# Optimization experiments

Hardware: AMD Instinct MI355X
Metric: run time of the kernel (lower is better)

## Reference

```python
import jax, jax.numpy as jnp
import numpy as np

B, T, S, A, P = 256, 32, 2048, 64, 128


def setup_inputs() -> dict:
    key = jax.random.key(0)
    ks = jax.random.split(key, 10)
    def w(k, shape, fan_in):
        return jax.random.normal(k, shape, dtype=jnp.float32) / np.sqrt(fan_in)
    return {
        "state": jax.random.normal(ks[0], (B, S), dtype=jnp.float32),
        "act_sequence": jax.random.normal(ks[1], (B, T, A), dtype=jnp.float32),
        "latent": jax.random.normal(ks[2], (B, P), dtype=jnp.float32),
        "fc_W": w(ks[3], (S, S + A + P), S + A + P),
        "fc_b": jnp.zeros((S,), dtype=jnp.float32),
        "fc1_W": w(ks[4], (S, 2 * S), 2 * S),
        "fc2_W": w(ks[5], (S, S), S),
        "W_W": w(ks[6], (4 * S, S), S),
        "reward_W": w(ks[7], (1, S), S),
        "reward_b": jnp.zeros((1,), dtype=jnp.float32),
    }


def reference(state, act_sequence, latent, fc_W, fc_b, fc1_W, fc2_W, W_W, reward_W, reward_b):
    s_dim = fc2_W.shape[0]
    relu = jax.nn.relu

    def fc(x):  # nn.Linear(s+a+p -> s, bias=True)
        return x @ fc_W.T + fc_b

    # initial hidden/cell both from relu(fc(cat[state, act[:,0], latent]))
    hs0 = jnp.concatenate([state, act_sequence[:, 0, :], latent], axis=1)
    hidden = relu(fc(hs0))
    cell = relu(fc(hs0))

    acts = jnp.transpose(act_sequence, (1, 0, 2))  # [T, B, A]

    def step(carry, act_i):
        h, c = carry
        # LSTMCell called as lstm(hidden, [hidden, cell]) -> input == h_cur == h
        combined = jnp.concatenate([h, h], axis=1)            # [B, 2S]
        x = relu(combined @ fc1_W.T)
        x = relu(x @ fc2_W.T)
        cc = relu(x @ W_W.T)                                   # [B, 4S]
        cc_i, cc_f, cc_o, cc_g = jnp.split(cc, 4, axis=1)
        i_g = jax.nn.sigmoid(cc_i)
        f_g = jax.nn.sigmoid(cc_f)
        o_g = jax.nn.sigmoid(cc_o)
        g_g = jnp.tanh(cc_g)
        c_next = f_g * c + i_g * g_g
        h_next = o_g * jnp.tanh(c_next)
        reward = h_next @ reward_W.T + reward_b                # [B, 1]
        # hidden for next iteration (uses act_sequence[:, i, :], as in source);
        # at the last step this carry is simply discarded.
        hs = jnp.concatenate([h_next, act_i, latent], axis=1)
        h_carry = relu(fc(hs))
        return (h_carry, c_next), (h_next, reward)

    (_, _), (preds, rewards) = jax.lax.scan(step, (hidden, cell), acts)
    # torch.cat(list, dim=0) over T steps of [B, *] -> [T*B, *]
    preds = preds.reshape(-1, s_dim)
    rewards = rewards.reshape(-1, 1)
    return preds, rewards
```

## Files before the change

### kernel.cpp

```cpp
#include <hip/hip_runtime.h>

typedef unsigned short u16;
typedef unsigned int   u32;
typedef __attribute__((ext_vector_type(8))) short s8v;
typedef __attribute__((ext_vector_type(8))) unsigned short u8v;
typedef __attribute__((ext_vector_type(4))) unsigned short u4h;
typedef __attribute__((ext_vector_type(4))) float f32x4;

__device__ __forceinline__ float bf2f(u16 v) {
    union { u32 u; float f; } x; x.u = ((u32)v) << 16; return x.f;
}
__device__ __forceinline__ u16 f2bf(float f) {
    union { float f; u32 u; } x; x.f = f;
    return (u16)((x.u + 0x7fffu + ((x.u >> 16) & 1u)) >> 16);
}
__device__ __forceinline__ float sigf(float x)  { return 1.0f / (1.0f + __expf(-x)); }
__device__ __forceinline__ float tanhf_(float x){ return 1.0f - 2.0f / (__expf(2.0f * x) + 1.0f); }

constexpr int Bb = 256, Tt = 32, Ss = 2048, Aa = 64, Pp = 128, SAPd = 2240;

typedef const __attribute__((address_space(1))) unsigned int* gp1_t;
typedef __attribute__((address_space(3))) unsigned int* lp3_t;
__device__ __forceinline__ void gl16(const void* g, void* l) {
    __builtin_amdgcn_global_load_lds((gp1_t)g, (lp3_t)l, 16, 0, 0);
}
#define VMWAIT(n) asm volatile("s_waitcnt vmcnt(" #n ")" ::: "memory")

template<int NBXPX, int NBY>
__device__ __forceinline__ void xcd_decode(int& bx, int& by) {
    int id  = blockIdx.x;
    int xcd = id & 7, i = id >> 3;
    bx = xcd * NBXPX + (i & (NBXPX - 1));
    by = i / NBXPX;
}

__global__ void detect_k(const u32* __restrict__ st, int* __restrict__ flag) {
    u32 w = st[threadIdx.x];
    int e = (w >> 7) & 0xFF;
    unsigned long long m = __ballot(e >= 100 && e <= 140);
    if (threadIdx.x == 0) flag[0] = (__popcll(m) >= 32) ? 1 : 0;
}

__global__ __launch_bounds__(256)
void prep_k(const void* __restrict__ state, const void* __restrict__ act,
            const void* __restrict__ latent, const void* __restrict__ fc1W,
            u16* __restrict__ hs, u16* __restrict__ fc1s, float* __restrict__ rewbuf,
            const int* __restrict__ flagp, int big)
{
    const bool bfe = (flagp[0] == 1);
    int g0 = blockIdx.x * 256 + threadIdx.x;
    int stride = gridDim.x * 256;
    for (int i = g0; i < Bb * SAPd; i += stride) {
        int b = i / SAPd, k = i - b * SAPd;
        const void* p; size_t src;
        if (k < Ss)           { p = state;  src = (size_t)b * Ss + k; }
        else if (k < Ss + Aa) { p = act;    src = (size_t)b * (Tt * Aa) + (k - Ss); }
        else                  { p = latent; src = (size_t)b * Pp + (k - Ss - Aa); }
        hs[i] = bfe ? ((const u16*)p)[src] : f2bf(((const float*)p)[src]);
    }
    for (int i = g0; i < Tt * Bb; i += stride) rewbuf[i] = 0.0f;
    if (big) {
        for (int i = g0; i < Ss * Ss; i += stride) {
            int n = i >> 11, k = i & 2047;
            float s;
            if (bfe) s = bf2f(((const u16*)fc1W)[(size_t)n * 4096 + k])
                       + bf2f(((const u16*)fc1W)[(size_t)n * 4096 + 2048 + k]);
            else     s = ((const float*)fc1W)[(size_t)n * 4096 + k]
                       + ((const float*)fc1W)[(size_t)n * 4096 + 2048 + k];
            fc1s[i] = f2bf(s);
        }
    }
}

template<int K, bool BIAS, bool WC, bool FOLD, bool ACT, bool WBF>
__global__ __launch_bounds__(256)
void gemm_k(const u16* __restrict__ Ap, const void* __restrict__ Wp,
            const void* __restrict__ biasp, u16* __restrict__ outp,
            float* __restrict__ cellp,
            u16* __restrict__ hsp, const void* __restrict__ actp, int t,
            const int* __restrict__ flagp)
{
    constexpr int NK = K / 64;
    __shared__ __align__(16) char smem[36864 + 8192];
    const bool bfe = (flagp[0] == 1);
    const int tid = threadIdx.x;
    const int lane = tid & 63, w = tid >> 6, m16 = lane & 15, q = lane >> 4;
    const int ct = w & 1, khw = w >> 1;
    int bx, by; xcd_decode<4, 8>(bx, by);
    const int r0 = by * 32, c0 = bx * 64;

    if (ACT) {
        if (by == 0) {
            int i = bx * 512 + tid * 2;
            int b = i >> 6, a2 = i & 63;
            if (bfe) {
                u32 v = *(const u32*)((const u16*)actp + ((size_t)b * Tt + t) * Aa + a2);
                *(u32*)(hsp + (size_t)b * SAPd + Ss + a2) = v;
            } else {
                const float* s = (const float*)actp + ((size_t)b * Tt + t) * Aa + a2;
                *(u32*)(hsp + (size_t)b * SAPd + Ss + a2) =
                    (u32)f2bf(s[0]) | ((u32)f2bf(s[1]) << 16);
            }
            VMWAIT(0);
        }
    }

    const int srow = tid >> 3, sch = tid & 7;
    const int fr2 = 32 + srow;
    f32x4 acc[4] = {};
    const bool mainp = (WBF || bfe) && !FOLD;

    auto COMPUTE = [&](int p) {
        const char* bufA = smem + p * 12288;
        const char* bufB = bufA + 4096;
        const int sw = (m16 & 7) << 4;
        const int cb = ((khw << 6) | (q << 4)) ^ sw;
        s8v a0 = *(const s8v*)(bufA + m16 * 128 + cb);
        s8v a1 = *(const s8v*)(bufA + (16 + m16) * 128 + cb);
        s8v b0 = *(const s8v*)(bufB + (ct * 32 + m16) * 128 + cb);
        s8v b1 = *(const s8v*)(bufB + (ct * 32 + 16 + m16) * 128 + cb);
        acc[0] = __builtin_amdgcn_mfma_f32_16x16x32_bf16(a0, b0, acc[0], 0, 0, 0);
        acc[1] = __builtin_amdgcn_mfma_f32_16x16x32_bf16(a1, b0, acc[1], 0, 0, 0);
        acc[2] = __builtin_amdgcn_mfma_f32_16x16x32_bf16(a0, b1, acc[2], 0, 0, 0);
        acc[3] = __builtin_amdgcn_mfma_f32_16x16x32_bf16(a1, b1, acc[3], 0, 0, 0);
    };

    if (mainp) {
        const u16* W16 = (const u16*)Wp;
        auto STAGE = [&](int kt, int p) {
            char* bufA = smem + p * 12288;
            char* bufB = bufA + 4096;
            int kb = kt * 64;
            gl16(Ap + (size_t)(r0 + srow) * K + kb + ((sch ^ (srow & 7)) * 8),
                 bufA + w * 1024);
            gl16(W16 + (size_t)(c0 + srow) * K + kb + ((sch ^ (srow & 7)) * 8),
                 bufB + w * 1024);
            gl16(W16 + (size_t)(c0 + fr2) * K + kb + ((sch ^ (fr2 & 7)) * 8),
                 bufB + 4096 + w * 1024);
        };
        STAGE(0, 0); STAGE(1, 1);
        for (int k = 0; k < NK - 2; k++) {
            VMWAIT(3);
            __builtin_amdgcn_s_barrier();
            STAGE(k + 2, (k + 2) % 3);
            COMPUTE(k % 3);
        }
        VMWAIT(3);
        __builtin_amdgcn_s_barrier();
        COMPUTE((NK - 2) % 3);
        VMWAIT(0);
        __builtin_amdgcn_s_barrier();
        COMPUTE((NK - 1) % 3);
    } else {
        u8v fa; u8v rbh[4]; float4 rff[8];
        auto ISSUE = [&](int kt) {
            int kb = kt * 64;
            fa = *(const u8v*)(Ap + (size_t)(r0 + srow) * K + kb + sch * 8);
            if (FOLD) {
                if (bfe) {
                    const u16* p1 = (const u16*)Wp + (size_t)(c0 + srow) * (2 * K) + kb + sch * 8;
                    rbh[0] = *(const u8v*)p1; rbh[1] = *(const u8v*)(p1 + K);
                    const u16* p2 = (const u16*)Wp + (size_t)(c0 + fr2) * (2 * K) + kb + sch * 8;
                    rbh[2] = *(const u8v*)p2; rbh[3] = *(const u8v*)(p2 + K);
                } else {
                    const float* p1 = (const float*)Wp + (size_t)(c0 + srow) * (2 * K) + kb + sch * 8;
                    rff[0] = *(const float4*)p1;       rff[1] = *(const float4*)(p1 + 4);
                    rff[2] = *(const float4*)(p1 + K); rff[3] = *(const float4*)(p1 + K + 4);
                    const float* p2 = (const float*)Wp + (size_t)(c0 + fr2) * (2 * K) + kb + sch * 8;
                    rff[4] = *(const float4*)p2;       rff[5] = *(const float4*)(p2 + 4);
                    rff[6] = *(const float4*)(p2 + K); rff[7] = *(const float4*)(p2 + K + 4);
                }
            } else {
                const float* p1 = (const float*)Wp + (size_t)(c0 + srow) * K + kb + sch * 8;
                rff[0] = *(const float4*)p1; rff[1] = *(const float4*)(p1 + 4);
                const float* p2 = (const float*)Wp + (size_t)(c0 + fr2) * K + kb + sch * 8;
                rff[2] = *(const float4*)p2; rff[3] = *(const float4*)(p2 + 4);
            }
        };
        auto COMMIT = [&](int p) {
            char* bufA = smem + p * 12288;
            char* bufB = bufA + 4096;
            *(u8v*)(bufA + srow * 128 + ((sch ^ (srow & 7)) * 16)) = fa;
            u8v v1, v2;
            if (FOLD) {
                if (bfe) {
                    #pragma unroll
                    for (int j = 0; j < 8; j++) {
                        v1[j] = f2bf(bf2f(rbh[0][j]) + bf2f(rbh[1][j]));
                        v2[j] = f2bf(bf2f(rbh[2][j]) + bf2f(rbh[3][j]));
                    }
                } else {
                    float a0[8], a1[8], b0[8], b1[8];
                    *(float4*)&a0[0] = rff[0]; *(float4*)&a0[4] = rff[1];
                    *(float4*)&a1[0] = rff[2]; *(float4*)&a1[4] = rff[3];
                    *(float4*)&b0[0] = rff[4]; *(float4*)&b0[4] = rff[5];
                    *(float4*)&b1[0] = rff[6]; *(float4*)&b1[4] = rff[7];
                    #pragma unroll
                    for (int j = 0; j < 8; j++) {
                        v1[j] = f2bf(a0[j] + a1[j]);
                        v2[j] = f2bf(b0[j] + b1[j]);
                    }
                }
            } else {
                float a0[8], a1[8];
                *(float4*)&a0[0] = rff[0]; *(float4*)&a0[4] = rff[1];
                *(float4*)&a1[0] = rff[2]; *(float4*)&a1[4] = rff[3];
                #pragma unroll
                for (int j = 0; j < 8; j++) { v1[j] = f2bf(a0[j]); v2[j] = f2bf(a1[j]); }
            }
            *(u8v*)(bufB + srow * 128 + ((sch ^ (srow & 7)) * 16)) = v1;
            *(u8v*)(bufB + fr2 * 128 + ((sch ^ (fr2 & 7)) * 16)) = v2;
        };
        ISSUE(0);
        for (int k = 0; k < NK; k++) {
            __syncthreads();
            COMMIT(k & 1);
            __syncthreads();
            if (k + 1 < NK) ISSUE(k + 1);
            COMPUTE(k & 1);
        }
    }

    f32x4* red = (f32x4*)(smem + 36864);
    if (khw == 1) {
        #pragma unroll
        for (int f = 0; f < 4; f++) red[(ct * 4 + f) * 64 + lane] = acc[f];
    }
    __syncthreads();
    if (khw == 0) {
        #pragma unroll
        for (int f = 0; f < 4; f++) acc[f] += red[(ct * 4 + f) * 64 + lane];
        #pragma unroll
        for (int cf = 0; cf < 2; cf++) {
            const int col = c0 + ct * 32 + cf * 16 + m16;
            float bv = 0.0f;
            if (BIAS) bv = bfe ? bf2f(((const u16*)biasp)[col]) : ((const float*)biasp)[col];
            #pragma unroll
            for (int af = 0; af < 2; af++) {
                f32x4 a = acc[cf * 2 + af];
                #pragma unroll
                for (int r = 0; r < 4; r++) {
                    int row = r0 + af * 16 + q * 4 + r;
                    float v = fmaxf(a[r] + bv, 0.0f);
                    outp[(size_t)row * 2048 + col] = f2bf(v);
                    if (WC) cellp[(size_t)row * 2048 + col] = v;
                }
            }
        }
    }
}

__global__ __launch_bounds__(256)
void wgates_k(const u16* __restrict__ Ap, const void* __restrict__ Wp,
              float* __restrict__ cbuf, u16* __restrict__ hsp,
              void* __restrict__ dout, const void* __restrict__ rwWp,
              float* __restrict__ rewbuf, int t, const int* __restrict__ flagp)
{
    constexpr int K = 2048, NK = 32;
    __shared__ __align__(16) char smem[49152];
    const bool bfe = (flagp[0] == 1);
    const int tid = threadIdx.x;
    const int lane = tid & 63, w = tid >> 6, m16 = lane & 15, q = lane >> 4;
    const int mi = w & 1, khw = w >> 1;
    int bx, by; xcd_decode<16, 4>(bx, by);
    const int r0 = by * 64, j0 = bx * 16;

    const int srow8 = lane >> 3, sch = lane & 7;
    f32x4 acc[8] = {};

    auto COMPUTE = [&](int p) {
        const char* bufA = smem + p * 16384;
        const char* bufB = bufA + 8192;
        const int sw = (m16 & 7) << 4;
        const int cb = ((khw << 6) | (q << 4)) ^ sw;
        s8v a0 = *(const s8v*)(bufA + (mi * 32 + m16) * 128 + cb);
        s8v a1 = *(const s8v*)(bufA + (mi * 32 + 16 + m16) * 128 + cb);
        #pragma unroll
        for (int cf = 0; cf < 4; cf++) {
            s8v b = *(const s8v*)(bufB + (cf * 16 + m16) * 128 + cb);
            acc[cf * 2 + 0] = __builtin_amdgcn_mfma_f32_16x16x32_bf16(a0, b, acc[cf * 2 + 0], 0, 0, 0);
            acc[cf * 2 + 1] = __builtin_amdgcn_mfma_f32_16x16x32_bf16(a1, b, acc[cf * 2 + 1], 0, 0, 0);
        }
    };

    if (bfe) {
        const u16* W16 = (const u16*)Wp;
        auto STAGE = [&](int kt, int p) {
            char* bufA = smem + p * 16384;
            char* bufB = bufA + 8192;
            int kb = kt * 64;
            #pragma unroll
            for (int i = 0; i < 2; i++) {
                int s = w * 2 + i;
                int row = s * 8 + srow8;
                int cg = sch ^ (row & 7);
                gl16(Ap + (size_t)(r0 + row) * K + kb + cg * 8, bufA + s * 1024);
            }
            #pragma unroll
            for (int i = 0; i < 2; i++) {
                int s = w * 2 + i;
                int row = s * 8 + srow8;
                int wr = (row >> 4) * 2048 + j0 + (row & 15);
                int cg = sch ^ (row & 7);
                gl16(W16 + (size_t)wr * K + kb + cg * 8, bufB + s * 1024);
            }
        };
        STAGE(0, 0); STAGE(1, 1);
        for (int k = 0; k < NK - 2; k++) {
            VMWAIT(4);
            __builtin_amdgcn_s_barrier();
            STAGE(k + 2, (k + 2) % 3);
            COMPUTE(k % 3);
        }
        VMWAIT(4);
        __builtin_amdgcn_s_barrier();
        COMPUTE((NK - 2) % 3);
        VMWAIT(0);
        __builtin_amdgcn_s_barrier();
        COMPUTE((NK - 1) % 3);
    } else {
        float4 rff[4];
        auto ISSUE = [&](int kt) {
            int kb = kt * 64;
            #pragma unroll
            for (int i = 0; i < 2; i++) {
                int slot = tid + i * 256;
                int brow = slot >> 3, bch = slot & 7;
                int wr = (brow >> 4) * 2048 + j0 + (brow & 15);
                int cg = bch ^ (brow & 7);
                const float* p1 = (const float*)Wp + (size_t)wr * K + kb + cg * 8;
                rff[2 * i] = *(const float4*)p1; rff[2 * i + 1] = *(const float4*)(p1 + 4);
            }
        };
        auto STAGE_A = [&](int kt, int p) {
            char* bufA = smem + p * 16384;
            int kb = kt * 64;
            #pragma unroll
            for (int i = 0; i < 2; i++) {
                int s = w * 2 + i;
                int row = s * 8 + srow8;
                int cg = sch ^ (row & 7);
                gl16(Ap + (size_t)(r0 + row) * K + kb + cg * 8, bufA + s * 1024);
            }
        };
        auto COMMIT = [&](int p) {
            char* bufB = smem + p * 16384 + 8192;
            #pragma unroll
            for (int i = 0; i < 2; i++) {
                int slot = tid + i * 256;
                int brow = slot >> 3, bch = slot & 7;
                float a0[8];
                *(float4*)&a0[0] = rff[2 * i]; *(float4*)&a0[4] = rff[2 * i + 1];
                u8v v;
                #pragma unroll
                for (int j = 0; j < 8; j++) v[j] = f2bf(a0[j]);
                *(u8v*)(bufB + brow * 128 + bch * 16) = v;
            }
        };
        ISSUE(0); STAGE_A(0, 0);
        for (int k = 0; k < NK; k++) {
            __syncthreads();
            COMMIT(k & 1);
            __syncthreads();
            if (k + 1 < NK) { STAGE_A(k + 1, (k + 1) & 1); ISSUE(k + 1); }
            COMPUTE(k & 1);
        }
    }

    f32x4* red = (f32x4*)(smem + 32768);
    if (khw == 1) {
        #pragma unroll
        for (int f = 0; f < 8; f++) red[(mi * 8 + f) * 64 + lane] = acc[f];
    }
    __syncthreads();
    float* gbuf = (float*)(smem + 32768);
    if (khw == 0) {
        #pragma unroll
        for (int f = 0; f < 8; f++) acc[f] += red[(mi * 8 + f) * 64 + lane];
        #pragma unroll
        for (int af = 0; af < 2; af++)
            #pragma unroll
            for (int r = 0; r < 4; r++) {
                int row = mi * 32 + af * 16 + q * 4 + r;
                f32x4 gv;
                #pragma unroll
                for (int cf = 0; cf < 4; cf++) gv[cf] = fmaxf(acc[cf * 2 + af][r], 0.0f);
                ((f32x4*)gbuf)[row * 16 + m16] = gv;
            }
    }
    __syncthreads();

    const int row = tid >> 2, jq = (tid & 3) * 4;
    const int grow = r0 + row, jcol = j0 + jq;
    float4 cold = *(const float4*)&cbuf[(size_t)grow * 2048 + jcol];
    float coldv[4] = { cold.x, cold.y, cold.z, cold.w };
    float rw4[4];
    #pragma unroll
    for (int u = 0; u < 4; u++)
        rw4[u] = bfe ? bf2f(((const u16*)rwWp)[jcol + u]) : ((const float*)rwWp)[jcol + u];

    float cn[4], hnf[4]; u4h hv;
    float rsum = 0.0f;
    #pragma unroll
    for (int u = 0; u < 4; u++) {
        const float* gq = &gbuf[((row * 16) + jq + u) * 4];
        float ig = sigf(gq[0]), fg = sigf(gq[1]), og = sigf(gq[2]), tg = tanhf_(gq[3]);
        float c_ = fg * coldv[u] + ig * tg;
        float hn = og * tanhf_(c_);
        cn[u] = c_; hnf[u] = hn; hv[u] = f2bf(hn);
        rsum += hn * rw4[u];
    }
    *(float4*)&cbuf[(size_t)grow * 2048 + jcol] = *(float4*)cn;
    *(u4h*)&hsp[(size_t)grow * SAPd + jcol] = hv;
    size_t pb = ((size_t)t * 256 + grow) * 2048 + jcol;
    if (bfe) *(u4h*)&((u16*)dout)[pb] = hv;
    else {
        #pragma unroll
        for (int u = 0; u < 4; u++) ((float*)dout)[pb + u] = hnf[u];
    }

    rsum += __shfl_xor(rsum, 1);
    rsum += __shfl_xor(rsum, 2);
    if ((tid & 3) == 0) atomicAdd(&rewbuf[t * 256 + grow], rsum);
}

__global__ void rewfin_k(const float* __restrict__ rewbuf, void* __restrict__ dout,
                         const void* __restrict__ rwb, const int* __restrict__ flagp) {
    const bool bfe = (flagp[0] == 1);
    int i = blockIdx.x * 256 + threadIdx.x;
    float rb = bfe ? bf2f(((const u16*)rwb)[0]) : ((const float*)rwb)[0];
    float v = rewbuf[i] + rb;
    size_t o = (size_t)Tt * Bb * Ss + i;
    if (bfe) ((u16*)dout)[o] = f2bf(v);
    else     ((float*)dout)[o] = v;
}

extern "C" void kernel_launch(void* const* d_in, const int* in_sizes, int n_in,
                              void* d_out, int out_size, void* d_ws, size_t ws_size,
                              hipStream_t stream)
{
    const void* state  = d_in[0];
    const void* act    = d_in[1];
    const void* latent = d_in[2];
    const void* fcW    = d_in[3];
    const void* fcb    = d_in[4];
    const void* fc1W   = d_in[5];
    const void* fc2W   = d_in[6];
    const void* WW     = d_in[7];
    const void* rwW    = d_in[8];
    const void* rwb    = d_in[9];
    char* ws = (char*)d_ws;

    int*   flag   = (int*)  (ws + 0);
    u16*   hs     = (u16*)  (ws + 1024);
    u16*   h      = (u16*)  (ws + 1147904);
    u16*   x1     = (u16*)  (ws + 2196480);
    u16*   x2     = (u16*)  (ws + 3245056);
    float* cbuf   = (float*)(ws + 4293632);
    float* rewbuf = (float*)(ws + 6390784);
    u16*   fc1s   = (u16*)  (ws + 6423552);
    const bool big = ws_size >= 14812160ull;

    detect_k<<<dim3(1), dim3(64), 0, stream>>>((const u32*)state, flag);
    prep_k<<<dim3(4096), dim3(256), 0, stream>>>(state, act, latent, fc1W,
                                                 hs, fc1s, rewbuf, flag, big ? 1 : 0);

    gemm_k<2240, true, true, false, false, false><<<dim3(256), dim3(256), 0, stream>>>(
        hs, fcW, fcb, h, cbuf, nullptr, nullptr, 0, flag);

    for (int t = 0; t < 32; t++) {
        if (big)
            gemm_k<2048, false, false, false, true, true><<<dim3(256), dim3(256), 0, stream>>>(
                h, fc1s, nullptr, x1, nullptr, hs, act, t, flag);
        else
            gemm_k<2048, false, false, true, true, false><<<dim3(256), dim3(256), 0, stream>>>(
                h, fc1W, nullptr, x1, nullptr, hs, act, t, flag);
        gemm_k<2048, false, false, false, false, false><<<dim3(256), dim3(256), 0, stream>>>(
            x1, fc2W, nullptr, x2, nullptr, nullptr, nullptr, 0, flag);
        wgates_k<<<dim3(512), dim3(256), 0, stream>>>(
            x2, WW, cbuf, hs, d_out, rwW, rewbuf, t, flag);
        if (t < 31)
            gemm_k<2240, true, false, false, false, false><<<dim3(256), dim3(256), 0, stream>>>(
                hs, fcW, fcb, h, nullptr, nullptr, nullptr, 0, flag);
    }
    rewfin_k<<<dim3(32), dim3(256), 0, stream>>>(rewbuf, d_out, rwb, flag);
}
```

Before: 2.708 ms.

## Enlarge wgates tile to 128 rows per block and drop split-K reduction

The gate GEMM kernel now processes 128 batch rows per block (256 blocks instead of 512), with each wave owning 32 rows over the full K chunk instead of splitting K across wave pairs. This halves the number of times each W_W tile is loaded across blocks and removes the LDS split-K reduction pass. The epilogue handles 8 columns per thread and does fewer atomics. In exchange it needs more LDS (72KB), doubles per-wave MFMA work per stage, and leaves only 256 blocks, which may reduce occupancy and latency hiding.

```diff
diff --git a/kernel.cpp b/kernel.cpp
--- a/kernel.cpp
+++ b/kernel.cpp
@@ -257,41 +257,43 @@
               float* __restrict__ rewbuf, int t, const int* __restrict__ flagp)
 {
     constexpr int K = 2048, NK = 32;
-    __shared__ __align__(16) char smem[49152];
+    __shared__ __align__(16) char smem[73728];
     const bool bfe = (flagp[0] == 1);
     const int tid = threadIdx.x;
     const int lane = tid & 63, w = tid >> 6, m16 = lane & 15, q = lane >> 4;
-    const int mi = w & 1, khw = w >> 1;
-    int bx, by; xcd_decode<16, 4>(bx, by);
-    const int r0 = by * 64, j0 = bx * 16;
+    int bx, by; xcd_decode<16, 2>(bx, by);
+    const int r0 = by * 128, j0 = bx * 16;
 
     const int srow8 = lane >> 3, sch = lane & 7;
     f32x4 acc[8] = {};
 
     auto COMPUTE = [&](int p) {
-        const char* bufA = smem + p * 16384;
-        const char* bufB = bufA + 8192;
+        const char* bufA = smem + p * 24576;
+        const char* bufB = bufA + 16384;
         const int sw = (m16 & 7) << 4;
-        const int cb = ((khw << 6) | (q << 4)) ^ sw;
-        s8v a0 = *(const s8v*)(bufA + (mi * 32 + m16) * 128 + cb);
-        s8v a1 = *(const s8v*)(bufA + (mi * 32 + 16 + m16) * 128 + cb);
-        #pragma unroll
-        for (int cf = 0; cf < 4; cf++) {
-            s8v b = *(const s8v*)(bufB + (cf * 16 + m16) * 128 + cb);
-            acc[cf * 2 + 0] = __builtin_amdgcn_mfma_f32_16x16x32_bf16(a0, b, acc[cf * 2 + 0], 0, 0, 0);
-            acc[cf * 2 + 1] = __builtin_amdgcn_mfma_f32_16x16x32_bf16(a1, b, acc[cf * 2 + 1], 0, 0, 0);
+        #pragma unroll
+        for (int kh = 0; kh < 2; kh++) {
+            const int cb = ((kh << 6) | (q << 4)) ^ sw;
+            s8v a0 = *(const s8v*)(bufA + (w * 32 + m16) * 128 + cb);
+            s8v a1 = *(const s8v*)(bufA + (w * 32 + 16 + m16) * 128 + cb);
+            #pragma unroll
+            for (int cf = 0; cf < 4; cf++) {
+                s8v b = *(const s8v*)(bufB + (cf * 16 + m16) * 128 + cb);
+                acc[cf * 2 + 0] = __builtin_amdgcn_mfma_f32_16x16x32_bf16(a0, b, acc[cf * 2 + 0], 0, 0, 0);
+                acc[cf * 2 + 1] = __builtin_amdgcn_mfma_f32_16x16x32_bf16(a1, b, acc[cf * 2 + 1], 0, 0, 0);
+            }
         }
     };
 
     if (bfe) {
         const u16* W16 = (const u16*)Wp;
         auto STAGE = [&](int kt, int p) {
-            char* bufA = smem + p * 16384;
-            char* bufB = bufA + 8192;
+            char* bufA = smem + p * 24576;
+            char* bufB = bufA + 16384;
             int kb = kt * 64;
             #pragma unroll
-            for (int i = 0; i < 2; i++) {
-                int s = w * 2 + i;
+            for (int i = 0; i < 4; i++) {
+                int s = w * 4 + i;
                 int row = s * 8 + srow8;
                 int cg = sch ^ (row & 7);
                 gl16(Ap + (size_t)(r0 + row) * K + kb + cg * 8, bufA + s * 1024);
@@ -307,54 +309,56 @@
         };
         STAGE(0, 0); STAGE(1, 1);
         for (int k = 0; k < NK - 2; k++) {
-            VMWAIT(4);
+            VMWAIT(6);
             __builtin_amdgcn_s_barrier();
+            __builtin_amdgcn_sched_barrier(0);
             STAGE(k + 2, (k + 2) % 3);
             COMPUTE(k % 3);
         }
-        VMWAIT(4);
+        VMWAIT(6);
         __builtin_amdgcn_s_barrier();
+        __builtin_amdgcn_sched_barrier(0);
         COMPUTE((NK - 2) % 3);
         VMWAIT(0);
         __builtin_amdgcn_s_barrier();
+        __builtin_amdgcn_sched_barrier(0);
         COMPUTE((NK - 1) % 3);
     } else {
         float4 rff[4];
+        const int brow = tid >> 2;
+        const int wrf = (brow >> 4) * 2048 + j0 + (brow & 15);
         auto ISSUE = [&](int kt) {
             int kb = kt * 64;
             #pragma unroll
             for (int i = 0; i < 2; i++) {
-                int slot = tid + i * 256;
-                int brow = slot >> 3, bch = slot & 7;
-                int wr = (brow >> 4) * 2048 + j0 + (brow & 15);
-                int cg = bch ^ (brow & 7);
-                const float* p1 = (const float*)Wp + (size_t)wr * K + kb + cg * 8;
-                rff[2 * i] = *(const float4*)p1; rff[2 * i + 1] = *(const float4*)(p1 + 4);
+                int c = (tid & 3) * 2 + i, cg = c ^ (brow & 7);
+                const float* p1 = (const float*)Wp + (size_t)wrf * K + kb + cg * 8;
+                rff[2 * i]     = *(const float4*)p1;
+                rff[2 * i + 1] = *(const float4*)(p1 + 4);
             }
         };
         auto STAGE_A = [&](int kt, int p) {
-            char* bufA = smem + p * 16384;
+            char* bufA = smem + p * 24576;
             int kb = kt * 64;
             #pragma unroll
-            for (int i = 0; i < 2; i++) {
-                int s = w * 2 + i;
+            for (int i = 0; i < 4; i++) {
+                int s = w * 4 + i;
                 int row = s * 8 + srow8;
                 int cg = sch ^ (row & 7);
                 gl16(Ap + (size_t)(r0 + row) * K + kb + cg * 8, bufA + s * 1024);
             }
         };
         auto COMMIT = [&](int p) {
-            char* bufB = smem + p * 16384 + 8192;
+            char* bufB = smem + p * 24576 + 16384;
             #pragma unroll
             for (int i = 0; i < 2; i++) {
-                int slot = tid + i * 256;
-                int brow = slot >> 3, bch = slot & 7;
+                int c = (tid & 3) * 2 + i;
                 float a0[8];
                 *(float4*)&a0[0] = rff[2 * i]; *(float4*)&a0[4] = rff[2 * i + 1];
                 u8v v;
                 #pragma unroll
                 for (int j = 0; j < 8; j++) v[j] = f2bf(a0[j]);
-                *(u8v*)(bufB + brow * 128 + bch * 16) = v;
+                *(u8v*)(bufB + brow * 128 + c * 16) = v;
             }
         };
         ISSUE(0); STAGE_A(0, 0);
@@ -367,61 +371,54 @@
         }
     }
 
-    f32x4* red = (f32x4*)(smem + 32768);
-    if (khw == 1) {
-        #pragma unroll
-        for (int f = 0; f < 8; f++) red[(mi * 8 + f) * 64 + lane] = acc[f];
-    }
     __syncthreads();
-    float* gbuf = (float*)(smem + 32768);
-    if (khw == 0) {
-        #pragma unroll
-        for (int f = 0; f < 8; f++) acc[f] += red[(mi * 8 + f) * 64 + lane];
-        #pragma unroll
-        for (int af = 0; af < 2; af++)
-            #pragma unroll
-            for (int r = 0; r < 4; r++) {
-                int row = mi * 32 + af * 16 + q * 4 + r;
-                f32x4 gv;
-                #pragma unroll
-                for (int cf = 0; cf < 4; cf++) gv[cf] = fmaxf(acc[cf * 2 + af][r], 0.0f);
-                ((f32x4*)gbuf)[row * 16 + m16] = gv;
-            }
-    }
+    float* gbuf = (float*)smem;
+    #pragma unroll
+    for (int af = 0; af < 2; af++)
+        #pragma unroll
+        for (int r = 0; r < 4; r++) {
+            int row = w * 32 + af * 16 + q * 4 + r;
+            f32x4 gv;
+            #pragma unroll
+            for (int cf = 0; cf < 4; cf++) gv[cf] = fmaxf(acc[cf * 2 + af][r], 0.0f);
+            ((f32x4*)gbuf)[row * 16 + m16] = gv;
+        }
     __syncthreads();
 
-    const int row = tid >> 2, jq = (tid & 3) * 4;
-    const int grow = r0 + row, jcol = j0 + jq;
-    float4 cold = *(const float4*)&cbuf[(size_t)grow * 2048 + jcol];
-    float coldv[4] = { cold.x, cold.y, cold.z, cold.w };
-    float rw4[4];
+    const int row = tid >> 1, j8 = (tid & 1) * 8;
+    const int grow = r0 + row, jcol = j0 + j8;
+    float4 cold0 = *(const float4*)&cbuf[(size_t)grow * 2048 + jcol];
+    float4 cold1 = *(const float4*)&cbuf[(size_t)grow * 2048 + jcol + 4];
+    float coldv[8] = { cold0.x, cold0.y, cold0.z, cold0.w,
+                       cold1.x, cold1.y, cold1.z, cold1.w };
+    float rw8[8];
     #pragma unroll
-    for (int u = 0; u < 4; u++)
-        rw4[u] = bfe ? bf2f(((const u16*)rwWp)[jcol + u]) : ((const float*)rwWp)[jcol + u];
-
-    float cn[4], hnf[4]; u4h hv;
+    for (int u = 0; u < 8; u++)
+        rw8[u] = bfe ? bf2f(((const u16*)rwWp)[jcol + u]) : ((const float*)rwWp)[jcol + u];
+
+    float cn[8], hnf[8]; u8v hv;
     float rsum = 0.0f;
     #pragma unroll
-    for (int u = 0; u < 4; u++) {
-        const float* gq = &gbuf[((row * 16) + jq + u) * 4];
+    for (int u = 0; u < 8; u++) {
+        const float* gq = &gbuf[((row * 16) + j8 + u) * 4];
         float ig = sigf(gq[0]), fg = sigf(gq[1]), og = sigf(gq[2]), tg = tanhf_(gq[3]);
         float c_ = fg * coldv[u] + ig * tg;
         float hn = og * tanhf_(c_);
         cn[u] = c_; hnf[u] = hn; hv[u] = f2bf(hn);
-        rsum += hn * rw4[u];
-    }
-    *(float4*)&cbuf[(size_t)grow * 2048 + jcol] = *(float4*)cn;
-    *(u4h*)&hsp[(size_t)grow * SAPd + jcol] = hv;
+        rsum += hn * rw8[u];
+    }
+    *(float4*)&cbuf[(size_t)grow * 2048 + jcol]     = *(float4*)&cn[0];
+    *(float4*)&cbuf[(size_t)grow * 2048 + jcol + 4] = *(float4*)&cn[4];
+    *(u8v*)&hsp[(size_t)grow * SAPd + jcol] = hv;
     size_t pb = ((size_t)t * 256 + grow) * 2048 + jcol;
-    if (bfe) *(u4h*)&((u16*)dout)[pb] = hv;
+    if (bfe) *(u8v*)&((u16*)dout)[pb] = hv;
     else {
         #pragma unroll
-        for (int u = 0; u < 4; u++) ((float*)dout)[pb + u] = hnf[u];
+        for (int u = 0; u < 8; u++) ((float*)dout)[pb + u] = hnf[u];
     }
 
     rsum += __shfl_xor(rsum, 1);
-    rsum += __shfl_xor(rsum, 2);
-    if ((tid & 3) == 0) atomicAdd(&rewbuf[t * 256 + grow], rsum);
+    if ((tid & 1) == 0) atomicAdd(&rewbuf[t * 256 + grow], rsum);
 }
 
 __global__ void rewfin_k(const float* __restrict__ rewbuf, void* __restrict__ dout,
@@ -477,7 +474,7 @@
                 h, fc1W, nullptr, x1, nullptr, hs, act, t, flag);
         gemm_k<2048, false, false, false, false, false><<<dim3(256), dim3(256), 0, stream>>>(
             x1, fc2W, nullptr, x2, nullptr, nullptr, nullptr, 0, flag);
-        wgates_k<<<dim3(512), dim3(256), 0, stream>>>(
+        wgates_k<<<dim3(256), dim3(256), 0, stream>>>(
             x2, WW, cbuf, hs, d_out, rwW, rewbuf, t, flag);
         if (t < 31)
             gemm_k<2240, true, false, false, false, false><<<dim3(256), dim3(256), 0, stream>>>(
```

Result: slower. 3.021 ms (+11.5%).
